# Kernel tuning notes

Measured on AMD Instinct MI355X. Metric: run time of the kernel, lower is better.

The kernel has to match this reference:

```python
import jax, jax.numpy as jnp
import numpy as np

EPS = 1e-5
NEG_INF = float('-inf')

B, L, D = 4, 1024, 1024
H = 16
HD = D // H
I = 3280  # _round_to_multiple(3.2 * 1024, 8)
WIN = 256
STD = 0.01


def rmsnorm(x, w):
    x = jnp.clip(x.astype(jnp.float32), -10000.0, 10000.0)
    rms = jnp.sqrt(jnp.maximum(jnp.mean(x * x, axis=-1, keepdims=True), EPS) + EPS)
    out = x / rms * w
    return jnp.where(jnp.isfinite(out), out, jnp.zeros_like(out))


def setup_inputs() -> dict:
    key = jax.random.key(0)
    ks = jax.random.split(key, 12)
    inp = {
        'x': jax.random.normal(ks[0], (B, L, D), dtype=jnp.float32),
        'wq_w': jax.random.normal(ks[1], (D, D), dtype=jnp.float32) * STD,
        'wq_b': jnp.zeros((D,), jnp.float32),
        'wk_w': jax.random.normal(ks[2], (D, D), dtype=jnp.float32) * STD,
        'wk_b': jnp.zeros((D,), jnp.float32),
        'wv_w': jax.random.normal(ks[3], (D, D), dtype=jnp.float32) * STD,
        'wv_b': jnp.zeros((D,), jnp.float32),
        'wo_w': jax.random.normal(ks[4], (D, D), dtype=jnp.float32) * STD,
        'wo_b': jnp.zeros((D,), jnp.float32),
        'q_norm_w': jnp.ones((HD,), jnp.float32),
        'k_norm_w': jnp.ones((HD,), jnp.float32),
        'seq_norm_w': jnp.ones((D,), jnp.float32),
        'seq_post_norm_w': jnp.ones((D,), jnp.float32),
        'ffn_norm_w': jnp.ones((D,), jnp.float32),
        'ffn_post_norm_w': jnp.ones((D,), jnp.float32),
        'w1_w': jax.random.normal(ks[5], (I, D), dtype=jnp.float32) * STD,
        'w1_b': jnp.zeros((I,), jnp.float32),
        'w2_w': jax.random.normal(ks[6], (D, I), dtype=jnp.float32) * STD,
        'w2_b': jnp.zeros((D,), jnp.float32),
        'w3_w': jax.random.normal(ks[7], (I, D), dtype=jnp.float32) * STD,
        'w3_b': jnp.zeros((I,), jnp.float32),
        'window_size': WIN,
    }
    return inp


def attention(x, wq_w, wq_b, wk_w, wk_b, wv_w, wv_b, wo_w, wo_b, q_norm_w, k_norm_w, window_size):
    b, l, d = x.shape
    x = x.astype(jnp.float32)
    q = (x @ wq_w.T + wq_b).reshape(b, l, H, HD)
    k = (x @ wk_w.T + wk_b).reshape(b, l, H, HD)
    v = (x @ wv_w.T + wv_b).reshape(b, l, H, HD)
    q = rmsnorm(q, q_norm_w)
    k = rmsnorm(k, k_norm_w)
    scale = HD ** -0.5
    scores = jnp.einsum('blhd,bmhd->bhlm', q, k) * scale
    i = jnp.arange(l)[:, None]
    j = jnp.arange(l)[None, :]
    masked = (j > i) | (i - j >= window_size)  # True => forbidden
    scores = scores + jnp.where(masked, NEG_INF, 0.0)
    p = jax.nn.softmax(scores, axis=-1)
    attn = jnp.einsum('bhlm,bmhd->blhd', p, v)
    attn = jnp.where(jnp.isfinite(attn), attn, jnp.zeros_like(attn))
    attn = attn.reshape(b, l, d)
    return attn @ wo_w.T + wo_b


def swiglu(x, w1_w, w1_b, w2_w, w2_b, w3_w, w3_b):
    x = x.astype(jnp.float32)
    z1 = x @ w1_w.T + w1_b
    z3 = x @ w3_w.T + w3_b
    return (jax.nn.silu(z1) * z3) @ w2_w.T + w2_b


def reference(x, wq_w, wq_b, wk_w, wk_b, wv_w, wv_b, wo_w, wo_b,
              q_norm_w, k_norm_w, seq_norm_w, seq_post_norm_w,
              ffn_norm_w, ffn_post_norm_w,
              w1_w, w1_b, w2_w, w2_b, w3_w, w3_b, window_size):
    # seq_norm -> attn -> seq_post_norm -> residual
    a = attention(rmsnorm(x, seq_norm_w), wq_w, wq_b, wk_w, wk_b, wv_w, wv_b,
                  wo_w, wo_b, q_norm_w, k_norm_w, window_size)
    h = x + rmsnorm(a, seq_post_norm_w)
    # ffn_norm -> ffn -> ffn_post_norm -> residual
    f = swiglu(rmsnorm(h, ffn_norm_w), w1_w, w1_b, w2_w, w2_b, w3_w, w3_b)
    return h + rmsnorm(f, ffn_post_norm_w)
```

## Files before the change

### kernel.cpp

```cpp
#include <hip/hip_runtime.h>
#include <cmath>
#include <cstdint>

typedef __bf16 bf16;
typedef bf16 bf16x4 __attribute__((ext_vector_type(4)));
typedef bf16 bf16x8 __attribute__((ext_vector_type(8)));
typedef float f32x4 __attribute__((ext_vector_type(4)));
typedef unsigned int u32;
typedef u32 u32x4 __attribute__((ext_vector_type(4)));

#define EPS 1e-5f

__device__ __forceinline__ float clipf(float v) {
    return fminf(fmaxf(v, -10000.0f), 10000.0f);
}
__device__ __forceinline__ float fin0(float v) { return isfinite(v) ? v : 0.0f; }

__device__ __forceinline__ void async_copy16(void* lds, const void* g) {
    __builtin_amdgcn_global_load_lds((__attribute__((address_space(1))) void*)(void*)g,
                                     (__attribute__((address_space(3))) void*)lds,
                                     16, 0, 0);
}

__global__ __launch_bounds__(256) void prep(const float* __restrict__ wq, const float* __restrict__ wk,
                                            const float* __restrict__ wv, const float* __restrict__ wo,
                                            bf16* __restrict__ Wq, bf16* __restrict__ Wk,
                                            bf16* __restrict__ Wv, bf16* __restrict__ Wo,
                                            const float* __restrict__ w1, const float* __restrict__ w3,
                                            bf16* __restrict__ W1p, bf16* __restrict__ W3p,
                                            const float* __restrict__ w2, bf16* __restrict__ W2p,
                                            const float* __restrict__ x, const float* __restrict__ snw,
                                            bf16* __restrict__ xn) {
    const int bid = blockIdx.x, t = threadIdx.x;
    if (bid < 4096) {
        int z = bid >> 10, r = bid & 1023;
        const float* in = (z == 0) ? wq : (z == 1) ? wk : (z == 2) ? wv : wo;
        bf16* out = (z == 0) ? Wq : (z == 1) ? Wk : (z == 2) ? Wv : Wo;
        f32x4 v = ((const f32x4*)(in + (size_t)r * 1024))[t];
        bf16x4 o = {(bf16)v[0], (bf16)v[1], (bf16)v[2], (bf16)v[3]};
        ((bf16x4*)(out + (size_t)r * 1024))[t] = o;
    } else if (bid < 10752) {
        int b2 = bid - 4096;
        int which = b2 >= 3328;
        int r = b2 - (which ? 3328 : 0);
        const float* in = which ? w3 : w1;
        bf16* out = which ? W3p : W1p;
        bf16x4 o = {(bf16)0.f, (bf16)0.f, (bf16)0.f, (bf16)0.f};
        if (r < 3280) {
            f32x4 v = ((const f32x4*)(in + (size_t)r * 1024))[t];
            o[0] = (bf16)v[0]; o[1] = (bf16)v[1]; o[2] = (bf16)v[2]; o[3] = (bf16)v[3];
        }
        ((bf16x4*)(out + (size_t)r * 1024))[t] = o;
    } else if (bid < 11776) {
        int r = bid - 10752;
        for (int c4 = t * 4; c4 < 3328; c4 += 1024) {
            bf16x4 o = {(bf16)0.f, (bf16)0.f, (bf16)0.f, (bf16)0.f};
            if (c4 + 3 < 3280) {
                f32x4 v = *(const f32x4*)(w2 + (size_t)r * 3280 + c4);
                o[0] = (bf16)v[0]; o[1] = (bf16)v[1]; o[2] = (bf16)v[2]; o[3] = (bf16)v[3];
            } else {
                #pragma unroll
                for (int j = 0; j < 4; ++j)
                    if (c4 + j < 3280) o[j] = (bf16)w2[(size_t)r * 3280 + c4 + j];
            }
            *(bf16x4*)(W2p + (size_t)r * 3328 + c4) = o;
        }
    } else {
        __shared__ float sred[4];
        int row = bid - 11776;
        f32x4 xv = ((const f32x4*)(x + (size_t)row * 1024))[t];
        f32x4 cv;
        cv[0] = clipf(xv[0]); cv[1] = clipf(xv[1]); cv[2] = clipf(xv[2]); cv[3] = clipf(xv[3]);
        float ss = cv[0]*cv[0] + cv[1]*cv[1] + cv[2]*cv[2] + cv[3]*cv[3];
        #pragma unroll
        for (int off = 32; off >= 1; off >>= 1) ss += __shfl_xor(ss, off, 64);
        if ((t & 63) == 0) sred[t >> 6] = ss;
        __syncthreads();
        float tot = sred[0] + sred[1] + sred[2] + sred[3];
        float rms = sqrtf(fmaxf(tot * (1.0f / 1024.0f), EPS) + EPS);
        f32x4 wv_ = ((const f32x4*)snw)[t];
        bf16x4 o;
        o[0] = (bf16)fin0(cv[0] / rms * wv_[0]);
        o[1] = (bf16)fin0(cv[1] / rms * wv_[1]);
        o[2] = (bf16)fin0(cv[2] / rms * wv_[2]);
        o[3] = (bf16)fin0(cv[3] / rms * wv_[3]);
        *(bf16x4*)(xn + (size_t)row * 1024 + t * 4) = o;
    }
}

__global__ __launch_bounds__(256) void gemm_qkv(const bf16* __restrict__ A,
                                                const bf16* __restrict__ B0,
                                                const bf16* __restrict__ B1,
                                                const bf16* __restrict__ B2,
                                                const float* __restrict__ g0,
                                                const float* __restrict__ g1,
                                                const float* __restrict__ g2,
                                                const float* __restrict__ qnw,
                                                const float* __restrict__ knw,
                                                bf16* __restrict__ C0,
                                                bf16* __restrict__ C1,
                                                bf16* __restrict__ VT) {
    const int z = blockIdx.z;
    const bf16* B = (z == 0) ? B0 : (z == 1) ? B1 : B2;
    const float* bias = (z == 0) ? g0 : (z == 1) ? g1 : g2;
    const float* hw = (z == 0) ? qnw : knw;

    __shared__ __align__(16) bf16 sA[2][128 * 32];
    __shared__ __align__(16) bf16 sB[2][128 * 32];
    const int tid = threadIdx.x;
    const int w = tid >> 6, lane = tid & 63;
    const int m0 = blockIdx.x * 128;
    const int n0 = blockIdx.y * 128;
    const int mwo = (w >> 1) * 64, nwo = (w & 1) * 64;
    const int r16 = lane & 15, quad = lane >> 4;
    const int kreg = quad * 8;
    const int K = 1024, N = 1024;

    f32x4 zero = {0.f, 0.f, 0.f, 0.f};
    f32x4 acc[4][4];
    #pragma unroll
    for (int i = 0; i < 4; ++i)
        #pragma unroll
        for (int j = 0; j < 4; ++j) acc[i][j] = zero;

    const int c0 = tid, c1 = tid + 256;
    const int am0 = c0 >> 2, ak0 = (c0 & 3) << 3;
    const int am1 = c1 >> 2, ak1 = (c1 & 3) << 3;

    {
        async_copy16(&sA[0][c0 * 8], &A[(size_t)(m0 + am0) * K + ak0]);
        async_copy16(&sA[0][c1 * 8], &A[(size_t)(m0 + am1) * K + ak1]);
        async_copy16(&sB[0][c0 * 8], &B[(size_t)(n0 + am0) * K + ak0]);
        async_copy16(&sB[0][c1 * 8], &B[(size_t)(n0 + am1) * K + ak1]);
    }
    for (int kt = 0; kt < 32; ++kt) {
        __syncthreads();
        const int cur = kt & 1, nxt = cur ^ 1;
        if (kt + 1 < 32) {
            const int kb = (kt + 1) << 5;
            async_copy16(&sA[nxt][c0 * 8], &A[(size_t)(m0 + am0) * K + kb + ak0]);
            async_copy16(&sA[nxt][c1 * 8], &A[(size_t)(m0 + am1) * K + kb + ak1]);
            async_copy16(&sB[nxt][c0 * 8], &B[(size_t)(n0 + am0) * K + kb + ak0]);
            async_copy16(&sB[nxt][c1 * 8], &B[(size_t)(n0 + am1) * K + kb + ak1]);
        }
        bf16x8 af[4], bfr[4];
        #pragma unroll
        for (int i = 0; i < 4; ++i) {
            af[i]  = *(const bf16x8*)&sA[cur][(mwo + i * 16 + r16) * 32 + kreg];
            bfr[i] = *(const bf16x8*)&sB[cur][(nwo + i * 16 + r16) * 32 + kreg];
        }
        #pragma unroll
        for (int mi = 0; mi < 4; ++mi)
            #pragma unroll
            for (int ni = 0; ni < 4; ++ni)
                acc[mi][ni] = __builtin_amdgcn_mfma_f32_16x16x32_bf16(af[mi], bfr[ni], acc[mi][ni], 0, 0, 0);
    }

    float bv[4];
    #pragma unroll
    for (int ni = 0; ni < 4; ++ni) bv[ni] = bias[n0 + nwo + ni * 16 + r16];

    if (z < 2) {
        bf16* C = (z == 0) ? C0 : C1;
        float nwv[4];
        #pragma unroll
        for (int ni = 0; ni < 4; ++ni) nwv[ni] = hw[ni * 16 + r16];
        #pragma unroll
        for (int mi = 0; mi < 4; ++mi) {
            #pragma unroll
            for (int r = 0; r < 4; ++r) {
                float v[4], ss = 0.0f;
                #pragma unroll
                for (int ni = 0; ni < 4; ++ni) {
                    v[ni] = clipf(acc[mi][ni][r] + bv[ni]);
                    ss += v[ni] * v[ni];
                }
                ss += __shfl_xor(ss, 1, 64);
                ss += __shfl_xor(ss, 2, 64);
                ss += __shfl_xor(ss, 4, 64);
                ss += __shfl_xor(ss, 8, 64);
                float rms = sqrtf(fmaxf(ss * (1.0f / 64.0f), EPS) + EPS);
                int row = m0 + mwo + mi * 16 + quad * 4 + r;
                #pragma unroll
                for (int ni = 0; ni < 4; ++ni) {
                    int col = n0 + nwo + ni * 16 + r16;
                    C[(size_t)row * N + col] = (bf16)fin0(v[ni] / rms * nwv[ni]);
                }
            }
        }
    } else {
        const int b_ = m0 >> 10;
        const int tokbase = (m0 & 1023) + mwo;
        #pragma unroll
        for (int ni = 0; ni < 4; ++ni) {
            int col = n0 + nwo + ni * 16 + r16;
            int h_ = col >> 6, hd = col & 63;
            bf16* dst = VT + (((size_t)b_ * 16 + h_) * 64 + hd) * 1024;
            #pragma unroll
            for (int mi = 0; mi < 4; ++mi) {
                bf16x4 pack;
                #pragma unroll
                for (int r = 0; r < 4; ++r) pack[r] = (bf16)(acc[mi][ni][r] + bv[ni]);
                *(bf16x4*)&dst[tokbase + mi * 16 + quad * 4] = pack;
            }
        }
    }
}

__global__ __launch_bounds__(256) void attn_win(const bf16* __restrict__ q,
                                                const bf16* __restrict__ k,
                                                const bf16* __restrict__ vt,
                                                const int* __restrict__ winp,
                                                bf16* __restrict__ o) {
    __shared__ __align__(16) bf16 sQ[64 * 64];
    __shared__ __align__(16) bf16 sK[64 * 64];
    __shared__ __align__(16) bf16 sVt[64 * 80];
    __shared__ __align__(16) bf16 sP[64 * 64];
    const int tid = threadIdx.x, w = tid >> 6, lane = tid & 63;
    const int qt = blockIdx.x, h = blockIdx.y, b = blockIdx.z;
    const int q0 = qt * 64;
    const int win = *winp;
    const float scale = 0.125f;
    const int r16 = lane & 15, quad = lane >> 4;

    {
        int qr0 = tid >> 3, col0 = (tid & 7) * 8;
        async_copy16(&sQ[tid * 8], &q[(((size_t)b * 1024 + q0 + qr0) * 16 + h) * 64 + col0]);
        int c1 = tid + 256;
        int qr1 = c1 >> 3, col1 = (c1 & 7) * 8;
        async_copy16(&sQ[c1 * 8], &q[(((size_t)b * 1024 + q0 + qr1) * 16 + h) * 64 + col1]);
    }
    __syncthreads();
    bf16x8 aq0 = *(const bf16x8*)&sQ[(w * 16 + r16) * 64 + quad * 8];
    bf16x8 aq1 = *(const bf16x8*)&sQ[(w * 16 + r16) * 64 + 32 + quad * 8];

    float Lr[4];
    f32x4 zero = {0.f, 0.f, 0.f, 0.f};
    f32x4 accO[4];
    #pragma unroll
    for (int r = 0; r < 4; ++r) Lr[r] = 0.0f;
    #pragma unroll
    for (int nf = 0; nf < 4; ++nf) accO[nf] = zero;

    int lo = q0 - (win - 1); if (lo < 0) lo = 0;
    const int kt0 = lo >> 6;
    const bf16* vth = vt + ((size_t)b * 16 + h) * 64 * 1024;

    for (int kt = kt0; kt <= qt; ++kt) {
        __syncthreads();
        {
            int col0 = (tid & 7) * 8;
            async_copy16(&sK[tid * 8], &k[(((size_t)b * 1024 + kt * 64 + (tid >> 3)) * 16 + h) * 64 + col0]);
            int c1 = tid + 256;
            int col1 = (c1 & 7) * 8;
            async_copy16(&sK[c1 * 8], &k[(((size_t)b * 1024 + kt * 64 + (c1 >> 3)) * 16 + h) * 64 + col1]);
        }
        #pragma unroll
        for (int c = tid; c < 512; c += 256) {
            int hd = c >> 3, koff = (c & 7) * 8;
            *(u32x4*)&sVt[hd * 80 + koff] = *(const u32x4*)&vth[(size_t)hd * 1024 + kt * 64 + koff];
        }
        __syncthreads();

        f32x4 sf[4];
        #pragma unroll
        for (int nf = 0; nf < 4; ++nf) {
            bf16x8 bk0 = *(const bf16x8*)&sK[(nf * 16 + r16) * 64 + quad * 8];
            bf16x8 bk1 = *(const bf16x8*)&sK[(nf * 16 + r16) * 64 + 32 + quad * 8];
            f32x4 accS = zero;
            accS = __builtin_amdgcn_mfma_f32_16x16x32_bf16(aq0, bk0, accS, 0, 0, 0);
            accS = __builtin_amdgcn_mfma_f32_16x16x32_bf16(aq1, bk1, accS, 0, 0, 0);
            sf[nf] = accS;
        }

        #pragma unroll
        for (int r = 0; r < 4; ++r) {
            int i = q0 + w * 16 + quad * 4 + r;
            float ps = 0.0f;
            #pragma unroll
            for (int nf = 0; nf < 4; ++nf) {
                int j = kt * 64 + nf * 16 + r16;
                bool ok = (j <= i) && (i - j < win);
                float pv = ok ? __expf(sf[nf][r] * scale - 8.0f) : 0.0f;
                ps += pv;
                sP[(w * 16 + quad * 4 + r) * 64 + nf * 16 + r16] = (bf16)pv;
            }
            Lr[r] += ps;
        }
        __syncthreads();

        bf16x8 ap0 = *(const bf16x8*)&sP[(w * 16 + r16) * 64 + quad * 8];
        bf16x8 ap1 = *(const bf16x8*)&sP[(w * 16 + r16) * 64 + 32 + quad * 8];
        #pragma unroll
        for (int nf = 0; nf < 4; ++nf) {
            bf16x8 bv0 = *(const bf16x8*)&sVt[(nf * 16 + r16) * 80 + quad * 8];
            bf16x8 bv1 = *(const bf16x8*)&sVt[(nf * 16 + r16) * 80 + 32 + quad * 8];
            accO[nf] = __builtin_amdgcn_mfma_f32_16x16x32_bf16(ap0, bv0, accO[nf], 0, 0, 0);
            accO[nf] = __builtin_amdgcn_mfma_f32_16x16x32_bf16(ap1, bv1, accO[nf], 0, 0, 0);
        }
    }

    #pragma unroll
    for (int r = 0; r < 4; ++r) {
        float l = Lr[r];
        l += __shfl_xor(l, 1, 64);
        l += __shfl_xor(l, 2, 64);
        l += __shfl_xor(l, 4, 64);
        l += __shfl_xor(l, 8, 64);
        float inv = (l > 0.0f) ? 1.0f / l : 0.0f;
        int row = q0 + w * 16 + quad * 4 + r;
        #pragma unroll
        for (int nf = 0; nf < 4; ++nf) {
            float ov = fin0(accO[nf][r] * inv);
            o[(((size_t)b * 1024 + row) * 16 + h) * 64 + nf * 16 + r16] = (bf16)ov;
        }
    }
}

__global__ __launch_bounds__(512) void gemm_sk2(const bf16* __restrict__ A,
                                                const bf16* __restrict__ B,
                                                float* __restrict__ P,
                                                int K, int Kh) {
    __shared__ __align__(16) bf16 sA[2][256 * 32];
    __shared__ __align__(16) bf16 sB[2][128 * 32];
    const int tid = threadIdx.x;
    const int w = tid >> 6, lane = tid & 63;
    const int m0 = blockIdx.x * 256, n0 = blockIdx.y * 128;
    const int mwo = (w & 3) * 64, nwo = (w >> 2) * 64;
    const int r16 = lane & 15, quad = lane >> 4, kreg = quad * 8;
    const int kbase = blockIdx.z * Kh;
    const int N = 1024;

    const int ar0 = tid >> 2,        ak0 = (tid & 3) << 3;
    const int c1 = tid + 512;
    const int ar1 = c1 >> 2,         ak1 = (c1 & 3) << 3;
    const int br = tid >> 2,         bk = (tid & 3) << 3;

    f32x4 zero = {0.f, 0.f, 0.f, 0.f};
    f32x4 acc[4][4];
    #pragma unroll
    for (int i = 0; i < 4; ++i)
        #pragma unroll
        for (int j = 0; j < 4; ++j) acc[i][j] = zero;

    {
        async_copy16(&sA[0][tid * 8], &A[(size_t)(m0 + ar0) * K + kbase + ak0]);
        async_copy16(&sA[0][c1 * 8],  &A[(size_t)(m0 + ar1) * K + kbase + ak1]);
        async_copy16(&sB[0][tid * 8], &B[(size_t)(n0 + br) * K + kbase + bk]);
    }
    const int kIters = Kh >> 5;
    for (int kt = 0; kt < kIters; ++kt) {
        __syncthreads();
        const int cur = kt & 1, nxt = cur ^ 1;
        if (kt + 1 < kIters) {
            const int kb = kbase + ((kt + 1) << 5);
            async_copy16(&sA[nxt][tid * 8], &A[(size_t)(m0 + ar0) * K + kb + ak0]);
            async_copy16(&sA[nxt][c1 * 8],  &A[(size_t)(m0 + ar1) * K + kb + ak1]);
            async_copy16(&sB[nxt][tid * 8], &B[(size_t)(n0 + br) * K + kb + bk]);
        }
        bf16x8 af[4], bfr[4];
        #pragma unroll
        for (int i = 0; i < 4; ++i) {
            af[i]  = *(const bf16x8*)&sA[cur][(mwo + i * 16 + r16) * 32 + kreg];
            bfr[i] = *(const bf16x8*)&sB[cur][(nwo + i * 16 + r16) * 32 + kreg];
        }
        #pragma unroll
        for (int mi = 0; mi < 4; ++mi)
            #pragma unroll
            for (int ni = 0; ni < 4; ++ni)
                acc[mi][ni] = __builtin_amdgcn_mfma_f32_16x16x32_bf16(af[mi], bfr[ni], acc[mi][ni], 0, 0, 0);
    }

    float* Pz = P + (size_t)blockIdx.z * 4096 * 1024;
    #pragma unroll
    for (int mi = 0; mi < 4; ++mi)
        #pragma unroll
        for (int ni = 0; ni < 4; ++ni) {
            int col = n0 + nwo + ni * 16 + r16;
            #pragma unroll
            for (int r = 0; r < 4; ++r) {
                int row = m0 + mwo + mi * 16 + quad * 4 + r;
                Pz[(size_t)row * N + col] = acc[mi][ni][r];
            }
        }
}

template <bool EMIT>
__global__ __launch_bounds__(512) void resid_norm(const float* __restrict__ xres,
                                                  const float* __restrict__ p0,
                                                  const float* __restrict__ p1,
                                                  const float* __restrict__ bias,
                                                  const float* __restrict__ wpost,
                                                  const float* __restrict__ wnext,
                                                  float* __restrict__ hout,
                                                  bf16* __restrict__ hnout) {
    __shared__ float sred[8];
    const int tid = threadIdx.x;
    const int grp = tid >> 8, t = tid & 255;
    const int w4 = (tid >> 6) & 3;
    for (int it = 0; it < 4; ++it) {
        int row = it * 1024 + blockIdx.x * 2 + grp;
        f32x4 a0 = ((const f32x4*)(p0 + (size_t)row * 1024))[t];
        f32x4 a1 = ((const f32x4*)(p1 + (size_t)row * 1024))[t];
        f32x4 bv = ((const f32x4*)bias)[t];
        f32x4 af;
        af[0] = clipf(a0[0] + a1[0] + bv[0]);
        af[1] = clipf(a0[1] + a1[1] + bv[1]);
        af[2] = clipf(a0[2] + a1[2] + bv[2]);
        af[3] = clipf(a0[3] + a1[3] + bv[3]);
        float ss = af[0]*af[0] + af[1]*af[1] + af[2]*af[2] + af[3]*af[3];
        #pragma unroll
        for (int off = 32; off >= 1; off >>= 1) ss += __shfl_xor(ss, off, 64);
        __syncthreads();
        if ((tid & 63) == 0) sred[grp * 4 + w4] = ss;
        __syncthreads();
        float tot = sred[grp*4+0] + sred[grp*4+1] + sred[grp*4+2] + sred[grp*4+3];
        float rms1 = sqrtf(fmaxf(tot * (1.0f / 1024.0f), EPS) + EPS);
        f32x4 xv = ((const f32x4*)(xres + (size_t)row * 1024))[t];
        f32x4 wp = ((const f32x4*)wpost)[t];
        f32x4 hv;
        hv[0] = xv[0] + fin0(af[0] / rms1 * wp[0]);
        hv[1] = xv[1] + fin0(af[1] / rms1 * wp[1]);
        hv[2] = xv[2] + fin0(af[2] / rms1 * wp[2]);
        hv[3] = xv[3] + fin0(af[3] / rms1 * wp[3]);
        ((f32x4*)(hout + (size_t)row * 1024))[t] = hv;
        if (EMIT) {
            f32x4 cv;
            cv[0] = clipf(hv[0]); cv[1] = clipf(hv[1]); cv[2] = clipf(hv[2]); cv[3] = clipf(hv[3]);
            float ss2 = cv[0]*cv[0] + cv[1]*cv[1] + cv[2]*cv[2] + cv[3]*cv[3];
            #pragma unroll
            for (int off = 32; off >= 1; off >>= 1) ss2 += __shfl_xor(ss2, off, 64);
            __syncthreads();
            if ((tid & 63) == 0) sred[grp * 4 + w4] = ss2;
            __syncthreads();
            float tot2 = sred[grp*4+0] + sred[grp*4+1] + sred[grp*4+2] + sred[grp*4+3];
            float rms2 = sqrtf(fmaxf(tot2 * (1.0f / 1024.0f), EPS) + EPS);
            f32x4 wn = ((const f32x4*)wnext)[t];
            bf16x4 o;
            o[0] = (bf16)fin0(cv[0] / rms2 * wn[0]);
            o[1] = (bf16)fin0(cv[1] / rms2 * wn[1]);
            o[2] = (bf16)fin0(cv[2] / rms2 * wn[2]);
            o[3] = (bf16)fin0(cv[3] / rms2 * wn[3]);
            *(bf16x4*)(hnout + (size_t)row * 1024 + t * 4) = o;
        }
    }
}

__global__ __launch_bounds__(512) void gemm_ffn1(const bf16* __restrict__ A,
                                                 const bf16* __restrict__ B1,
                                                 const bf16* __restrict__ B3,
                                                 const float* __restrict__ b1,
                                                 const float* __restrict__ b3,
                                                 bf16* __restrict__ G) {
    __shared__ __align__(16) bf16 sA[2][128 * 32];
    __shared__ __align__(16) bf16 sB1[2][128 * 32];
    __shared__ __align__(16) bf16 sB3[2][128 * 32];
    const int tid = threadIdx.x;
    const int w = tid >> 6, lane = tid & 63;
    const int m0 = blockIdx.x * 128;
    const int n0 = blockIdx.y * 128;
    const int mwo = (w >> 2) * 64, nwo = (w & 3) * 32;
    const int r16 = lane & 15, quad = lane >> 4;
    const int kreg = quad * 8;
    const int K = 1024, N = 3328;

    f32x4 zero = {0.f, 0.f, 0.f, 0.f};
    f32x4 acc1[4][2], acc3[4][2];
    #pragma unroll
    for (int i = 0; i < 4; ++i)
        #pragma unroll
        for (int j = 0; j < 2; ++j) { acc1[i][j] = zero; acc3[i][j] = zero; }

    const int arow = tid >> 2, akoff = (tid & 3) << 3;

    {
        async_copy16(&sA[0][tid * 8],  &A[(size_t)(m0 + arow) * K + akoff]);
        async_copy16(&sB1[0][tid * 8], &B1[(size_t)(n0 + arow) * K + akoff]);
        async_copy16(&sB3[0][tid * 8], &B3[(size_t)(n0 + arow) * K + akoff]);
    }
    for (int kt = 0; kt < 32; ++kt) {
        __syncthreads();
        const int cur = kt & 1, nxt = cur ^ 1;
        if (kt + 1 < 32) {
            const int kb = (kt + 1) << 5;
            async_copy16(&sA[nxt][tid * 8],  &A[(size_t)(m0 + arow) * K + kb + akoff]);
            async_copy16(&sB1[nxt][tid * 8], &B1[(size_t)(n0 + arow) * K + kb + akoff]);
            async_copy16(&sB3[nxt][tid * 8], &B3[(size_t)(n0 + arow) * K + kb + akoff]);
        }
        bf16x8 af[4], bf1[2], bf3[2];
        #pragma unroll
        for (int i = 0; i < 4; ++i)
            af[i]  = *(const bf16x8*)&sA[cur][(mwo + i * 16 + r16) * 32 + kreg];
        #pragma unroll
        for (int i = 0; i < 2; ++i) {
            bf1[i] = *(const bf16x8*)&sB1[cur][(nwo + i * 16 + r16) * 32 + kreg];
            bf3[i] = *(const bf16x8*)&sB3[cur][(nwo + i * 16 + r16) * 32 + kreg];
        }
        #pragma unroll
        for (int mi = 0; mi < 4; ++mi)
            #pragma unroll
            for (int ni = 0; ni < 2; ++ni) {
                acc1[mi][ni] = __builtin_amdgcn_mfma_f32_16x16x32_bf16(af[mi], bf1[ni], acc1[mi][ni], 0, 0, 0);
                acc3[mi][ni] = __builtin_amdgcn_mfma_f32_16x16x32_bf16(af[mi], bf3[ni], acc3[mi][ni], 0, 0, 0);
            }
    }

    #pragma unroll
    for (int ni = 0; ni < 2; ++ni) {
        int col = n0 + nwo + ni * 16 + r16;
        float bv1 = (col < 3280) ? b1[col] : 0.0f;
        float bv3 = (col < 3280) ? b3[col] : 0.0f;
        #pragma unroll
        for (int mi = 0; mi < 4; ++mi) {
            #pragma unroll
            for (int r = 0; r < 4; ++r) {
                int row = m0 + mwo + mi * 16 + quad * 4 + r;
                float z1 = acc1[mi][ni][r] + bv1;
                float z3 = acc3[mi][ni][r] + bv3;
                float s = z1 / (1.0f + __expf(-z1));
                G[(size_t)row * N + col] = (bf16)(s * z3);
            }
        }
    }
}

extern "C" void kernel_launch(void* const* d_in, const int* in_sizes, int n_in,
                              void* d_out, int out_size, void* d_ws, size_t ws_size,
                              hipStream_t stream) {
    const float* x       = (const float*)d_in[0];
    const float* wq_w    = (const float*)d_in[1];
    const float* wq_b    = (const float*)d_in[2];
    const float* wk_w    = (const float*)d_in[3];
    const float* wk_b    = (const float*)d_in[4];
    const float* wv_w    = (const float*)d_in[5];
    const float* wv_b    = (const float*)d_in[6];
    const float* wo_w    = (const float*)d_in[7];
    const float* wo_b    = (const float*)d_in[8];
    const float* q_norm_w= (const float*)d_in[9];
    const float* k_norm_w= (const float*)d_in[10];
    const float* seq_norm_w      = (const float*)d_in[11];
    const float* seq_post_norm_w = (const float*)d_in[12];
    const float* ffn_norm_w      = (const float*)d_in[13];
    const float* ffn_post_norm_w = (const float*)d_in[14];
    const float* w1_w    = (const float*)d_in[15];
    const float* w1_b    = (const float*)d_in[16];
    const float* w2_w    = (const float*)d_in[17];
    const float* w2_b    = (const float*)d_in[18];
    const float* w3_w    = (const float*)d_in[19];
    const float* w3_b    = (const float*)d_in[20];
    const int*   winp    = (const int*)d_in[21];
    float* out = (float*)d_out;

    const size_t SZ_W   = 2097152;
    const size_t SZ_WP  = 6815744;
    const size_t SZ_ACT = 8388608;
    const size_t SZ_H   = 16777216;
    const size_t SZ_P   = 33554432;

    char* p = (char*)d_ws;
    bf16* Wq  = (bf16*)p; p += SZ_W;
    bf16* Wk  = (bf16*)p; p += SZ_W;
    bf16* Wv  = (bf16*)p; p += SZ_W;
    bf16* Wo  = (bf16*)p; p += SZ_W;
    bf16* W1p = (bf16*)p; p += SZ_WP;
    bf16* W3p = (bf16*)p; p += SZ_WP;
    bf16* W2p = (bf16*)p; p += SZ_WP;
    float* h  = (float*)p; p += SZ_H;
    bf16* hn  = (bf16*)p; p += SZ_ACT;
    float* part = (float*)p; p += SZ_P;
    float* part1 = part + (size_t)4096 * 1024;
    char* regionA = p;
    bf16* xn    = (bf16*)(regionA);
    bf16* qb    = (bf16*)(regionA + 1 * SZ_ACT);
    bf16* kb    = (bf16*)(regionA + 2 * SZ_ACT);
    bf16* vtb   = (bf16*)(regionA + 3 * SZ_ACT);
    bf16* attnb = (bf16*)(regionA + 4 * SZ_ACT);
    bf16* g     = (bf16*)(regionA);

    prep<<<dim3(15872), dim3(256), 0, stream>>>(wq_w, wk_w, wv_w, wo_w, Wq, Wk, Wv, Wo,
                                                w1_w, w3_w, W1p, W3p, w2_w, W2p,
                                                x, seq_norm_w, xn);

    gemm_qkv<<<dim3(32, 8, 3), dim3(256), 0, stream>>>(xn, Wq, Wk, Wv, wq_b, wk_b, wv_b,
                                                       q_norm_w, k_norm_w, qb, kb, vtb);

    attn_win<<<dim3(16, 16, 4), dim3(256), 0, stream>>>(qb, kb, vtb, winp, attnb);

    gemm_sk2<<<dim3(16, 8, 2), dim3(512), 0, stream>>>(attnb, Wo, part, 1024, 512);

    resid_norm<true><<<dim3(512), dim3(512), 0, stream>>>(x, part, part1, wo_b,
                                                          seq_post_norm_w, ffn_norm_w, h, hn);

    gemm_ffn1<<<dim3(32, 26), dim3(512), 0, stream>>>(hn, W1p, W3p, w1_b, w3_b, g);

    gemm_sk2<<<dim3(16, 8, 2), dim3(512), 0, stream>>>(g, W2p, part, 3328, 1664);

    resid_norm<false><<<dim3(512), dim3(512), 0, stream>>>(h, part, part1, w2_b,
                                                           ffn_post_norm_w, nullptr, out, nullptr);
}
```

Baseline: 371.0 us.

## Interleave W1/W3 weights and rewrite FFN1 GEMM with 256x256 tiles and phased pipeline

The prep kernel now interleaves W1 and W3 rows in blocks of 16 into one combined weight matrix, so FFN1 runs as a single GEMM with N=6656. The new FFN1 kernel uses 256x256 block tiles with K-tiles of 64, XOR-swizzled LDS layout, staggered async loads for A and B halves interleaved with MFMA phases, s_setprio around MFMA bursts, and a grouped block-index swizzle for L2 locality. It is meant to raise data reuse per LDS load and overlap global loads with compute, in exchange for more registers and LDS per block and hand-tuned waitcnt ordering that could be fragile.

```diff
diff --git a/kernel.cpp b/kernel.cpp
--- a/kernel.cpp
+++ b/kernel.cpp
@@ -27,7 +27,7 @@
                                             bf16* __restrict__ Wq, bf16* __restrict__ Wk,
                                             bf16* __restrict__ Wv, bf16* __restrict__ Wo,
                                             const float* __restrict__ w1, const float* __restrict__ w3,
-                                            bf16* __restrict__ W1p, bf16* __restrict__ W3p,
+                                            bf16* __restrict__ Wf,
                                             const float* __restrict__ w2, bf16* __restrict__ W2p,
                                             const float* __restrict__ x, const float* __restrict__ snw,
                                             bf16* __restrict__ xn) {
@@ -40,17 +40,15 @@
         bf16x4 o = {(bf16)v[0], (bf16)v[1], (bf16)v[2], (bf16)v[3]};
         ((bf16x4*)(out + (size_t)r * 1024))[t] = o;
     } else if (bid < 10752) {
-        int b2 = bid - 4096;
-        int which = b2 >= 3328;
-        int r = b2 - (which ? 3328 : 0);
-        const float* in = which ? w3 : w1;
-        bf16* out = which ? W3p : W1p;
+        int ri = bid - 4096;
+        int lc = ((ri >> 5) << 4) + (ri & 15);
+        const float* in = ((ri >> 4) & 1) ? w3 : w1;
         bf16x4 o = {(bf16)0.f, (bf16)0.f, (bf16)0.f, (bf16)0.f};
-        if (r < 3280) {
-            f32x4 v = ((const f32x4*)(in + (size_t)r * 1024))[t];
+        if (lc < 3280) {
+            f32x4 v = ((const f32x4*)(in + (size_t)lc * 1024))[t];
             o[0] = (bf16)v[0]; o[1] = (bf16)v[1]; o[2] = (bf16)v[2]; o[3] = (bf16)v[3];
         }
-        ((bf16x4*)(out + (size_t)r * 1024))[t] = o;
+        ((bf16x4*)(Wf + (size_t)ri * 1024))[t] = o;
     } else if (bid < 11776) {
         int r = bid - 10752;
         for (int c4 = t * 4; c4 < 3328; c4 += 1024) {
@@ -446,79 +444,119 @@
     }
 }
 
-__global__ __launch_bounds__(512) void gemm_ffn1(const bf16* __restrict__ A,
-                                                 const bf16* __restrict__ B1,
-                                                 const bf16* __restrict__ B3,
-                                                 const float* __restrict__ b1,
-                                                 const float* __restrict__ b3,
-                                                 bf16* __restrict__ G) {
-    __shared__ __align__(16) bf16 sA[2][128 * 32];
-    __shared__ __align__(16) bf16 sB1[2][128 * 32];
-    __shared__ __align__(16) bf16 sB3[2][128 * 32];
+template <int MB>
+__device__ __forceinline__ void mphase(const bf16* Ah, const bf16x8 (&breg)[4][2],
+                                       f32x4 (&acc)[8][4], int r16, int koff0, int koff1) {
+    const bf16* pa0 = &Ah[(MB * 16 + r16) * 64];
+    const bf16* pa1 = &Ah[((MB + 1) * 16 + r16) * 64];
+    bf16x8 a00 = *(const bf16x8*)&pa0[koff0];
+    bf16x8 a01 = *(const bf16x8*)&pa0[koff1];
+    bf16x8 a10 = *(const bf16x8*)&pa1[koff0];
+    bf16x8 a11 = *(const bf16x8*)&pa1[koff1];
+    __builtin_amdgcn_s_setprio(1);
+    #pragma unroll
+    for (int n = 0; n < 4; ++n) {
+        acc[MB][n]     = __builtin_amdgcn_mfma_f32_16x16x32_bf16(a00, breg[n][0], acc[MB][n], 0, 0, 0);
+        acc[MB][n]     = __builtin_amdgcn_mfma_f32_16x16x32_bf16(a01, breg[n][1], acc[MB][n], 0, 0, 0);
+        acc[MB + 1][n] = __builtin_amdgcn_mfma_f32_16x16x32_bf16(a10, breg[n][0], acc[MB + 1][n], 0, 0, 0);
+        acc[MB + 1][n] = __builtin_amdgcn_mfma_f32_16x16x32_bf16(a11, breg[n][1], acc[MB + 1][n], 0, 0, 0);
+    }
+    __builtin_amdgcn_s_setprio(0);
+}
+
+__global__ __launch_bounds__(512, 2) void gemm_ffn1_8ph(const bf16* __restrict__ A,
+                                                        const bf16* __restrict__ Wf,
+                                                        const float* __restrict__ b1,
+                                                        const float* __restrict__ b3,
+                                                        bf16* __restrict__ G) {
+    __shared__ __align__(16) bf16 sA[2][2][128 * 64];
+    __shared__ __align__(16) bf16 sB[2][2][128 * 64];
     const int tid = threadIdx.x;
     const int w = tid >> 6, lane = tid & 63;
-    const int m0 = blockIdx.x * 128;
-    const int n0 = blockIdx.y * 128;
-    const int mwo = (w >> 2) * 64, nwo = (w & 3) * 32;
+    const int wr = w >> 2, wc = w & 3;
     const int r16 = lane & 15, quad = lane >> 4;
-    const int kreg = quad * 8;
-    const int K = 1024, N = 3328;
-
-    f32x4 zero = {0.f, 0.f, 0.f, 0.f};
-    f32x4 acc1[4][2], acc3[4][2];
-    #pragma unroll
-    for (int i = 0; i < 4; ++i)
-        #pragma unroll
-        for (int j = 0; j < 2; ++j) { acc1[i][j] = zero; acc3[i][j] = zero; }
-
-    const int arow = tid >> 2, akoff = (tid & 3) << 3;
-
-    {
-        async_copy16(&sA[0][tid * 8],  &A[(size_t)(m0 + arow) * K + akoff]);
-        async_copy16(&sB1[0][tid * 8], &B1[(size_t)(n0 + arow) * K + akoff]);
-        async_copy16(&sB3[0][tid * 8], &B3[(size_t)(n0 + arow) * K + akoff]);
-    }
-    for (int kt = 0; kt < 32; ++kt) {
-        __syncthreads();
-        const int cur = kt & 1, nxt = cur ^ 1;
-        if (kt + 1 < 32) {
-            const int kb = (kt + 1) << 5;
-            async_copy16(&sA[nxt][tid * 8],  &A[(size_t)(m0 + arow) * K + kb + akoff]);
-            async_copy16(&sB1[nxt][tid * 8], &B1[(size_t)(n0 + arow) * K + kb + akoff]);
-            async_copy16(&sB3[nxt][tid * 8], &B3[(size_t)(n0 + arow) * K + kb + akoff]);
-        }
-        bf16x8 af[4], bf1[2], bf3[2];
-        #pragma unroll
-        for (int i = 0; i < 4; ++i)
-            af[i]  = *(const bf16x8*)&sA[cur][(mwo + i * 16 + r16) * 32 + kreg];
-        #pragma unroll
-        for (int i = 0; i < 2; ++i) {
-            bf1[i] = *(const bf16x8*)&sB1[cur][(nwo + i * 16 + r16) * 32 + kreg];
-            bf3[i] = *(const bf16x8*)&sB3[cur][(nwo + i * 16 + r16) * 32 + kreg];
-        }
-        #pragma unroll
-        for (int mi = 0; mi < 4; ++mi)
-            #pragma unroll
-            for (int ni = 0; ni < 2; ++ni) {
-                acc1[mi][ni] = __builtin_amdgcn_mfma_f32_16x16x32_bf16(af[mi], bf1[ni], acc1[mi][ni], 0, 0, 0);
-                acc3[mi][ni] = __builtin_amdgcn_mfma_f32_16x16x32_bf16(af[mi], bf3[ni], acc3[mi][ni], 0, 0, 0);
-            }
-    }
-
-    #pragma unroll
-    for (int ni = 0; ni < 2; ++ni) {
-        int col = n0 + nwo + ni * 16 + r16;
-        float bv1 = (col < 3280) ? b1[col] : 0.0f;
-        float bv3 = (col < 3280) ? b3[col] : 0.0f;
-        #pragma unroll
-        for (int mi = 0; mi < 4; ++mi) {
-            #pragma unroll
-            for (int r = 0; r < 4; ++r) {
-                int row = m0 + mwo + mi * 16 + quad * 4 + r;
-                float z1 = acc1[mi][ni][r] + bv1;
-                float z3 = acc3[mi][ni][r] + bv3;
+
+    const int flat = blockIdx.x;
+    const int swb = (flat & 7) * 52 + (flat >> 3);
+    const int bm = swb & 15, bn = swb >> 4;
+    const int m0 = bm * 256;
+    const int n0i = bn * 256;
+
+    const int swz = r16 & 7;
+    const int koff0 = ((quad ^ swz) << 3);
+    const int koff1 = (((quad + 4) ^ swz) << 3);
+
+    const int sr0 = tid >> 3, sr1 = sr0 + 64;
+    const int sk0 = (((tid & 7) ^ (sr0 & 7)) << 3);
+
+    const bf16* aSrc0 = A + (size_t)m0 * 1024;
+    const bf16* aSrc1 = A + (size_t)(m0 + 128) * 1024;
+    const bf16* bSrc0 = Wf + (size_t)n0i * 1024;
+    const bf16* bSrc1 = Wf + (size_t)(n0i + 128) * 1024;
+
+#define STAGE(dst, src, ktile) do {                                                        \
+        async_copy16(&(dst)[tid * 8],         (src) + (size_t)sr0 * 1024 + (ktile) * 64 + sk0); \
+        async_copy16(&(dst)[(tid + 512) * 8], (src) + (size_t)sr1 * 1024 + (ktile) * 64 + sk0); \
+    } while (0)
+
+    f32x4 acc[8][4];
+    #pragma unroll
+    for (int i = 0; i < 8; ++i)
+        #pragma unroll
+        for (int j = 0; j < 4; ++j) acc[i][j] = (f32x4){0.f, 0.f, 0.f, 0.f};
+
+    STAGE(sB[0][0], bSrc0, 0); STAGE(sB[0][1], bSrc1, 0);
+    STAGE(sA[0][0], aSrc0, 0); STAGE(sA[0][1], aSrc1, 0);
+    STAGE(sB[1][0], bSrc0, 1); STAGE(sB[1][1], bSrc1, 1);
+
+    for (int t = 0; t < 16; ++t) {
+        const int cur = t & 1, nxt = cur ^ 1;
+        const bf16* Ah = &sA[cur][wr][0];
+        const bf16* Bh = &sB[cur][wc >> 1][0];
+        const int rbB = (wc & 1) << 6;
+        bf16x8 breg[4][2];
+
+        __builtin_amdgcn_s_barrier();
+        if (t + 1 < 16) {
+            STAGE(sA[nxt][0], aSrc0, t + 1);
+            STAGE(sA[nxt][1], aSrc1, t + 1);
+        }
+        if (t == 15) { asm volatile("s_waitcnt vmcnt(0)" ::: "memory"); }
+        else         { asm volatile("s_waitcnt vmcnt(8)" ::: "memory"); }
+        #pragma unroll
+        for (int n = 0; n < 4; ++n) {
+            const bf16* p = &Bh[(rbB + n * 16 + r16) * 64];
+            breg[n][0] = *(const bf16x8*)&p[koff0];
+            breg[n][1] = *(const bf16x8*)&p[koff1];
+        }
+        mphase<0>(Ah, breg, acc, r16, koff0, koff1);
+
+        __builtin_amdgcn_s_barrier();
+        if (t + 2 < 16) STAGE(sB[cur][0], bSrc0, t + 2);
+        mphase<2>(Ah, breg, acc, r16, koff0, koff1);
+
+        __builtin_amdgcn_s_barrier();
+        if (t + 2 < 16) STAGE(sB[cur][1], bSrc1, t + 2);
+        mphase<4>(Ah, breg, acc, r16, koff0, koff1);
+
+        mphase<6>(Ah, breg, acc, r16, koff0, koff1);
+    }
+#undef STAGE
+
+    #pragma unroll
+    for (int m = 0; m < 8; ++m) {
+        #pragma unroll
+        for (int p = 0; p < 2; ++p) {
+            int col = (bn * 8 + wc * 2 + p) * 16 + r16;
+            float bb1 = (col < 3280) ? b1[col] : 0.0f;
+            float bb3 = (col < 3280) ? b3[col] : 0.0f;
+            #pragma unroll
+            for (int rr = 0; rr < 4; ++rr) {
+                int row = m0 + wr * 128 + m * 16 + quad * 4 + rr;
+                float z1 = acc[m][2 * p][rr] + bb1;
+                float z3 = acc[m][2 * p + 1][rr] + bb3;
                 float s = z1 / (1.0f + __expf(-z1));
-                G[(size_t)row * N + col] = (bf16)(s * z3);
+                G[(size_t)row * 3328 + col] = (bf16)(s * z3);
             }
         }
     }
@@ -562,8 +600,7 @@
     bf16* Wk  = (bf16*)p; p += SZ_W;
     bf16* Wv  = (bf16*)p; p += SZ_W;
     bf16* Wo  = (bf16*)p; p += SZ_W;
-    bf16* W1p = (bf16*)p; p += SZ_WP;
-    bf16* W3p = (bf16*)p; p += SZ_WP;
+    bf16* Wfp = (bf16*)p; p += 2 * SZ_WP;
     bf16* W2p = (bf16*)p; p += SZ_WP;
     float* h  = (float*)p; p += SZ_H;
     bf16* hn  = (bf16*)p; p += SZ_ACT;
@@ -578,7 +615,7 @@
     bf16* g     = (bf16*)(regionA);
 
     prep<<<dim3(15872), dim3(256), 0, stream>>>(wq_w, wk_w, wv_w, wo_w, Wq, Wk, Wv, Wo,
-                                                w1_w, w3_w, W1p, W3p, w2_w, W2p,
+                                                w1_w, w3_w, Wfp, w2_w, W2p,
                                                 x, seq_norm_w, xn);
 
     gemm_qkv<<<dim3(32, 8, 3), dim3(256), 0, stream>>>(xn, Wq, Wk, Wv, wq_b, wk_b, wv_b,
@@ -591,7 +628,7 @@
     resid_norm<true><<<dim3(512), dim3(512), 0, stream>>>(x, part, part1, wo_b,
                                                           seq_post_norm_w, ffn_norm_w, h, hn);
 
-    gemm_ffn1<<<dim3(32, 26), dim3(512), 0, stream>>>(hn, W1p, W3p, w1_b, w3_b, g);
+    gemm_ffn1_8ph<<<dim3(416), dim3(512), 0, stream>>>(hn, Wfp, w1_b, w3_b, g);
 
     gemm_sk2<<<dim3(16, 8, 2), dim3(512), 0, stream>>>(g, W2p, part, 3328, 1664);
 
```

Result: slower. 391.6 us (+5.5%).

## Overlap Wo/FFN weight conversion with QKV GEMM via extra grid slice

Applied to the files above, without the earlier changes.

Moves the fp32-to-bf16 conversion of Wo, W1, W3 and W2 out of the prep kernel into a new z=0 slice of the QKV GEMM grid. 256 blocks stride over the 8704 weight rows while the other slices run the QKV GEMM. This shrinks the prep kernel and lets the bandwidth-bound conversion run alongside compute-bound GEMM work. The risk is that the conversion blocks hold CUs and compete for memory bandwidth with the GEMM, and that the z indexing has to be remapped correctly for Q, K and V.

```diff
diff --git a/kernel.cpp b/kernel.cpp
--- a/kernel.cpp
+++ b/kernel.cpp
@@ -23,51 +23,22 @@
 }
 
 __global__ __launch_bounds__(256) void prep(const float* __restrict__ wq, const float* __restrict__ wk,
-                                            const float* __restrict__ wv, const float* __restrict__ wo,
+                                            const float* __restrict__ wv,
                                             bf16* __restrict__ Wq, bf16* __restrict__ Wk,
-                                            bf16* __restrict__ Wv, bf16* __restrict__ Wo,
-                                            const float* __restrict__ w1, const float* __restrict__ w3,
-                                            bf16* __restrict__ W1p, bf16* __restrict__ W3p,
-                                            const float* __restrict__ w2, bf16* __restrict__ W2p,
+                                            bf16* __restrict__ Wv,
                                             const float* __restrict__ x, const float* __restrict__ snw,
                                             bf16* __restrict__ xn) {
     const int bid = blockIdx.x, t = threadIdx.x;
-    if (bid < 4096) {
+    if (bid < 3072) {
         int z = bid >> 10, r = bid & 1023;
-        const float* in = (z == 0) ? wq : (z == 1) ? wk : (z == 2) ? wv : wo;
-        bf16* out = (z == 0) ? Wq : (z == 1) ? Wk : (z == 2) ? Wv : Wo;
+        const float* in = (z == 0) ? wq : (z == 1) ? wk : wv;
+        bf16* out = (z == 0) ? Wq : (z == 1) ? Wk : Wv;
         f32x4 v = ((const f32x4*)(in + (size_t)r * 1024))[t];
         bf16x4 o = {(bf16)v[0], (bf16)v[1], (bf16)v[2], (bf16)v[3]};
         ((bf16x4*)(out + (size_t)r * 1024))[t] = o;
-    } else if (bid < 10752) {
-        int b2 = bid - 4096;
-        int which = b2 >= 3328;
-        int r = b2 - (which ? 3328 : 0);
-        const float* in = which ? w3 : w1;
-        bf16* out = which ? W3p : W1p;
-        bf16x4 o = {(bf16)0.f, (bf16)0.f, (bf16)0.f, (bf16)0.f};
-        if (r < 3280) {
-            f32x4 v = ((const f32x4*)(in + (size_t)r * 1024))[t];
-            o[0] = (bf16)v[0]; o[1] = (bf16)v[1]; o[2] = (bf16)v[2]; o[3] = (bf16)v[3];
-        }
-        ((bf16x4*)(out + (size_t)r * 1024))[t] = o;
-    } else if (bid < 11776) {
-        int r = bid - 10752;
-        for (int c4 = t * 4; c4 < 3328; c4 += 1024) {
-            bf16x4 o = {(bf16)0.f, (bf16)0.f, (bf16)0.f, (bf16)0.f};
-            if (c4 + 3 < 3280) {
-                f32x4 v = *(const f32x4*)(w2 + (size_t)r * 3280 + c4);
-                o[0] = (bf16)v[0]; o[1] = (bf16)v[1]; o[2] = (bf16)v[2]; o[3] = (bf16)v[3];
-            } else {
-                #pragma unroll
-                for (int j = 0; j < 4; ++j)
-                    if (c4 + j < 3280) o[j] = (bf16)w2[(size_t)r * 3280 + c4 + j];
-            }
-            *(bf16x4*)(W2p + (size_t)r * 3328 + c4) = o;
-        }
     } else {
         __shared__ float sred[4];
-        int row = bid - 11776;
+        int row = bid - 3072;
         f32x4 xv = ((const f32x4*)(x + (size_t)row * 1024))[t];
         f32x4 cv;
         cv[0] = clipf(xv[0]); cv[1] = clipf(xv[1]); cv[2] = clipf(xv[2]); cv[3] = clipf(xv[3]);
@@ -99,15 +70,61 @@
                                                 const float* __restrict__ knw,
                                                 bf16* __restrict__ C0,
                                                 bf16* __restrict__ C1,
-                                                bf16* __restrict__ VT) {
+                                                bf16* __restrict__ VT,
+                                                const float* __restrict__ wo,
+                                                const float* __restrict__ w1,
+                                                const float* __restrict__ w3,
+                                                const float* __restrict__ w2,
+                                                bf16* __restrict__ Wo,
+                                                bf16* __restrict__ W1p,
+                                                bf16* __restrict__ W3p,
+                                                bf16* __restrict__ W2p) {
     const int z = blockIdx.z;
-    const bf16* B = (z == 0) ? B0 : (z == 1) ? B1 : B2;
-    const float* bias = (z == 0) ? g0 : (z == 1) ? g1 : g2;
-    const float* hw = (z == 0) ? qnw : knw;
+    const int tid = threadIdx.x;
+
+    if (z == 0) {
+        const int cid = blockIdx.y * 32 + blockIdx.x;
+        for (int u = cid; u < 8704; u += 256) {
+            if (u < 1024) {
+                f32x4 v = ((const f32x4*)(wo + (size_t)u * 1024))[tid];
+                bf16x4 o = {(bf16)v[0], (bf16)v[1], (bf16)v[2], (bf16)v[3]};
+                ((bf16x4*)(Wo + (size_t)u * 1024))[tid] = o;
+            } else if (u < 7680) {
+                int which = u >= 4352;
+                int r = u - (which ? 4352 : 1024);
+                const float* in = which ? w3 : w1;
+                bf16* out = which ? W3p : W1p;
+                bf16x4 o = {(bf16)0.f, (bf16)0.f, (bf16)0.f, (bf16)0.f};
+                if (r < 3280) {
+                    f32x4 v = ((const f32x4*)(in + (size_t)r * 1024))[tid];
+                    o[0] = (bf16)v[0]; o[1] = (bf16)v[1]; o[2] = (bf16)v[2]; o[3] = (bf16)v[3];
+                }
+                ((bf16x4*)(out + (size_t)r * 1024))[tid] = o;
+            } else {
+                int r = u - 7680;
+                for (int c4 = tid * 4; c4 < 3328; c4 += 1024) {
+                    bf16x4 o = {(bf16)0.f, (bf16)0.f, (bf16)0.f, (bf16)0.f};
+                    if (c4 + 3 < 3280) {
+                        f32x4 v = *(const f32x4*)(w2 + (size_t)r * 3280 + c4);
+                        o[0] = (bf16)v[0]; o[1] = (bf16)v[1]; o[2] = (bf16)v[2]; o[3] = (bf16)v[3];
+                    } else {
+                        #pragma unroll
+                        for (int j = 0; j < 4; ++j)
+                            if (c4 + j < 3280) o[j] = (bf16)w2[(size_t)r * 3280 + c4 + j];
+                    }
+                    *(bf16x4*)(W2p + (size_t)r * 3328 + c4) = o;
+                }
+            }
+        }
+        return;
+    }
+
+    const bf16* B = (z == 1) ? B0 : (z == 2) ? B1 : B2;
+    const float* bias = (z == 1) ? g0 : (z == 2) ? g1 : g2;
+    const float* hw = (z == 1) ? qnw : knw;
 
     __shared__ __align__(16) bf16 sA[2][128 * 32];
     __shared__ __align__(16) bf16 sB[2][128 * 32];
-    const int tid = threadIdx.x;
     const int w = tid >> 6, lane = tid & 63;
     const int m0 = blockIdx.x * 128;
     const int n0 = blockIdx.y * 128;
@@ -160,8 +177,8 @@
     #pragma unroll
     for (int ni = 0; ni < 4; ++ni) bv[ni] = bias[n0 + nwo + ni * 16 + r16];
 
-    if (z < 2) {
-        bf16* C = (z == 0) ? C0 : C1;
+    if (z < 3) {
+        bf16* C = (z == 1) ? C0 : C1;
         float nwv[4];
         #pragma unroll
         for (int ni = 0; ni < 4; ++ni) nwv[ni] = hw[ni * 16 + r16];
@@ -577,12 +594,13 @@
     bf16* attnb = (bf16*)(regionA + 4 * SZ_ACT);
     bf16* g     = (bf16*)(regionA);
 
-    prep<<<dim3(15872), dim3(256), 0, stream>>>(wq_w, wk_w, wv_w, wo_w, Wq, Wk, Wv, Wo,
-                                                w1_w, w3_w, W1p, W3p, w2_w, W2p,
-                                                x, seq_norm_w, xn);
-
-    gemm_qkv<<<dim3(32, 8, 3), dim3(256), 0, stream>>>(xn, Wq, Wk, Wv, wq_b, wk_b, wv_b,
-                                                       q_norm_w, k_norm_w, qb, kb, vtb);
+    prep<<<dim3(7168), dim3(256), 0, stream>>>(wq_w, wk_w, wv_w, Wq, Wk, Wv,
+                                               x, seq_norm_w, xn);
+
+    gemm_qkv<<<dim3(32, 8, 4), dim3(256), 0, stream>>>(xn, Wq, Wk, Wv, wq_b, wk_b, wv_b,
+                                                       q_norm_w, k_norm_w, qb, kb, vtb,
+                                                       wo_w, w1_w, w3_w, w2_w,
+                                                       Wo, W1p, W3p, W2p);
 
     attn_win<<<dim3(16, 16, 4), dim3(256), 0, stream>>>(qb, kb, vtb, winp, attnb);
 
```

Measured after the change: 393.6 us. 1.06x slower.

## Fuse Q/K/V projections into one GEMM kernel sharing the A tile

Applied to the files above, without the earlier changes.

Replaces the three-way z-split QKV GEMM with a single 512-thread kernel that loads each A tile once and multiplies it against the Q, K and V weight tiles together. Each of the 8 warps covers a 32x64 sub-tile with three accumulator sets. The goal is to cut redundant activation loads and the number of launched blocks. The cost is more LDS per block (four double-buffered tiles), more accumulator registers per thread, and only 256 blocks instead of 768, which may reduce occupancy and parallelism.

```diff
diff --git a/kernel.cpp b/kernel.cpp
--- a/kernel.cpp
+++ b/kernel.cpp
@@ -88,91 +88,96 @@
     }
 }
 
-__global__ __launch_bounds__(256) void gemm_qkv(const bf16* __restrict__ A,
-                                                const bf16* __restrict__ B0,
-                                                const bf16* __restrict__ B1,
-                                                const bf16* __restrict__ B2,
-                                                const float* __restrict__ g0,
-                                                const float* __restrict__ g1,
-                                                const float* __restrict__ g2,
-                                                const float* __restrict__ qnw,
-                                                const float* __restrict__ knw,
-                                                bf16* __restrict__ C0,
-                                                bf16* __restrict__ C1,
-                                                bf16* __restrict__ VT) {
-    const int z = blockIdx.z;
-    const bf16* B = (z == 0) ? B0 : (z == 1) ? B1 : B2;
-    const float* bias = (z == 0) ? g0 : (z == 1) ? g1 : g2;
-    const float* hw = (z == 0) ? qnw : knw;
-
+__global__ __launch_bounds__(512) void gemm_qkv3(const bf16* __restrict__ A,
+                                                 const bf16* __restrict__ Bq,
+                                                 const bf16* __restrict__ Bk,
+                                                 const bf16* __restrict__ Bv,
+                                                 const float* __restrict__ biq,
+                                                 const float* __restrict__ bik,
+                                                 const float* __restrict__ biv,
+                                                 const float* __restrict__ qnw,
+                                                 const float* __restrict__ knw,
+                                                 bf16* __restrict__ Cq,
+                                                 bf16* __restrict__ Ck,
+                                                 bf16* __restrict__ VT) {
     __shared__ __align__(16) bf16 sA[2][128 * 32];
-    __shared__ __align__(16) bf16 sB[2][128 * 32];
+    __shared__ __align__(16) bf16 sBq[2][128 * 32];
+    __shared__ __align__(16) bf16 sBk[2][128 * 32];
+    __shared__ __align__(16) bf16 sBv[2][128 * 32];
     const int tid = threadIdx.x;
     const int w = tid >> 6, lane = tid & 63;
     const int m0 = blockIdx.x * 128;
     const int n0 = blockIdx.y * 128;
-    const int mwo = (w >> 1) * 64, nwo = (w & 1) * 64;
+    const int mwo = (w >> 1) * 32;
+    const int nwo = (w & 1) * 64;
     const int r16 = lane & 15, quad = lane >> 4;
     const int kreg = quad * 8;
     const int K = 1024, N = 1024;
 
     f32x4 zero = {0.f, 0.f, 0.f, 0.f};
-    f32x4 acc[4][4];
-    #pragma unroll
-    for (int i = 0; i < 4; ++i)
-        #pragma unroll
-        for (int j = 0; j < 4; ++j) acc[i][j] = zero;
-
-    const int c0 = tid, c1 = tid + 256;
-    const int am0 = c0 >> 2, ak0 = (c0 & 3) << 3;
-    const int am1 = c1 >> 2, ak1 = (c1 & 3) << 3;
+    f32x4 aq[2][4], ak[2][4], av[2][4];
+    #pragma unroll
+    for (int i = 0; i < 2; ++i)
+        #pragma unroll
+        for (int j = 0; j < 4; ++j) { aq[i][j] = zero; ak[i][j] = zero; av[i][j] = zero; }
+
+    const int arow = tid >> 2, akoff = (tid & 3) << 3;
 
     {
-        async_copy16(&sA[0][c0 * 8], &A[(size_t)(m0 + am0) * K + ak0]);
-        async_copy16(&sA[0][c1 * 8], &A[(size_t)(m0 + am1) * K + ak1]);
-        async_copy16(&sB[0][c0 * 8], &B[(size_t)(n0 + am0) * K + ak0]);
-        async_copy16(&sB[0][c1 * 8], &B[(size_t)(n0 + am1) * K + ak1]);
+        async_copy16(&sA[0][tid * 8],  &A[(size_t)(m0 + arow) * K + akoff]);
+        async_copy16(&sBq[0][tid * 8], &Bq[(size_t)(n0 + arow) * K + akoff]);
+        async_copy16(&sBk[0][tid * 8], &Bk[(size_t)(n0 + arow) * K + akoff]);
+        async_copy16(&sBv[0][tid * 8], &Bv[(size_t)(n0 + arow) * K + akoff]);
     }
     for (int kt = 0; kt < 32; ++kt) {
         __syncthreads();
         const int cur = kt & 1, nxt = cur ^ 1;
         if (kt + 1 < 32) {
             const int kb = (kt + 1) << 5;
-            async_copy16(&sA[nxt][c0 * 8], &A[(size_t)(m0 + am0) * K + kb + ak0]);
-            async_copy16(&sA[nxt][c1 * 8], &A[(size_t)(m0 + am1) * K + kb + ak1]);
-            async_copy16(&sB[nxt][c0 * 8], &B[(size_t)(n0 + am0) * K + kb + ak0]);
-            async_copy16(&sB[nxt][c1 * 8], &B[(size_t)(n0 + am1) * K + kb + ak1]);
-        }
-        bf16x8 af[4], bfr[4];
+            async_copy16(&sA[nxt][tid * 8],  &A[(size_t)(m0 + arow) * K + kb + akoff]);
+            async_copy16(&sBq[nxt][tid * 8], &Bq[(size_t)(n0 + arow) * K + kb + akoff]);
+            async_copy16(&sBk[nxt][tid * 8], &Bk[(size_t)(n0 + arow) * K + kb + akoff]);
+            async_copy16(&sBv[nxt][tid * 8], &Bv[(size_t)(n0 + arow) * K + kb + akoff]);
+        }
+        bf16x8 af[2], bq_[4], bk_[4], bv_[4];
+        #pragma unroll
+        for (int i = 0; i < 2; ++i)
+            af[i] = *(const bf16x8*)&sA[cur][(mwo + i * 16 + r16) * 32 + kreg];
         #pragma unroll
         for (int i = 0; i < 4; ++i) {
-            af[i]  = *(const bf16x8*)&sA[cur][(mwo + i * 16 + r16) * 32 + kreg];
-            bfr[i] = *(const bf16x8*)&sB[cur][(nwo + i * 16 + r16) * 32 + kreg];
-        }
-        #pragma unroll
-        for (int mi = 0; mi < 4; ++mi)
-            #pragma unroll
-            for (int ni = 0; ni < 4; ++ni)
-                acc[mi][ni] = __builtin_amdgcn_mfma_f32_16x16x32_bf16(af[mi], bfr[ni], acc[mi][ni], 0, 0, 0);
-    }
-
-    float bv[4];
-    #pragma unroll
-    for (int ni = 0; ni < 4; ++ni) bv[ni] = bias[n0 + nwo + ni * 16 + r16];
-
-    if (z < 2) {
-        bf16* C = (z == 0) ? C0 : C1;
-        float nwv[4];
-        #pragma unroll
-        for (int ni = 0; ni < 4; ++ni) nwv[ni] = hw[ni * 16 + r16];
-        #pragma unroll
-        for (int mi = 0; mi < 4; ++mi) {
+            bq_[i] = *(const bf16x8*)&sBq[cur][(nwo + i * 16 + r16) * 32 + kreg];
+            bk_[i] = *(const bf16x8*)&sBk[cur][(nwo + i * 16 + r16) * 32 + kreg];
+            bv_[i] = *(const bf16x8*)&sBv[cur][(nwo + i * 16 + r16) * 32 + kreg];
+        }
+        #pragma unroll
+        for (int mi = 0; mi < 2; ++mi)
+            #pragma unroll
+            for (int ni = 0; ni < 4; ++ni) {
+                aq[mi][ni] = __builtin_amdgcn_mfma_f32_16x16x32_bf16(af[mi], bq_[ni], aq[mi][ni], 0, 0, 0);
+                ak[mi][ni] = __builtin_amdgcn_mfma_f32_16x16x32_bf16(af[mi], bk_[ni], ak[mi][ni], 0, 0, 0);
+                av[mi][ni] = __builtin_amdgcn_mfma_f32_16x16x32_bf16(af[mi], bv_[ni], av[mi][ni], 0, 0, 0);
+            }
+    }
+
+    float nwq[4], nwk[4], bvq[4], bvk[4], bvv[4];
+    #pragma unroll
+    for (int ni = 0; ni < 4; ++ni) {
+        int col = n0 + nwo + ni * 16 + r16;
+        bvq[ni] = biq[col]; bvk[ni] = bik[col]; bvv[ni] = biv[col];
+        nwq[ni] = qnw[ni * 16 + r16]; nwk[ni] = knw[ni * 16 + r16];
+    }
+    #pragma unroll
+    for (int s = 0; s < 2; ++s) {
+        bf16* C = s ? Ck : Cq;
+        #pragma unroll
+        for (int mi = 0; mi < 2; ++mi) {
             #pragma unroll
             for (int r = 0; r < 4; ++r) {
                 float v[4], ss = 0.0f;
                 #pragma unroll
                 for (int ni = 0; ni < 4; ++ni) {
-                    v[ni] = clipf(acc[mi][ni][r] + bv[ni]);
+                    float a = s ? ak[mi][ni][r] : aq[mi][ni][r];
+                    v[ni] = clipf(a + (s ? bvk[ni] : bvq[ni]));
                     ss += v[ni] * v[ni];
                 }
                 ss += __shfl_xor(ss, 1, 64);
@@ -184,11 +189,13 @@
                 #pragma unroll
                 for (int ni = 0; ni < 4; ++ni) {
                     int col = n0 + nwo + ni * 16 + r16;
-                    C[(size_t)row * N + col] = (bf16)fin0(v[ni] / rms * nwv[ni]);
+                    float nw = s ? nwk[ni] : nwq[ni];
+                    C[(size_t)row * N + col] = (bf16)fin0(v[ni] / rms * nw);
                 }
             }
         }
-    } else {
+    }
+    {
         const int b_ = m0 >> 10;
         const int tokbase = (m0 & 1023) + mwo;
         #pragma unroll
@@ -197,10 +204,10 @@
             int h_ = col >> 6, hd = col & 63;
             bf16* dst = VT + (((size_t)b_ * 16 + h_) * 64 + hd) * 1024;
             #pragma unroll
-            for (int mi = 0; mi < 4; ++mi) {
+            for (int mi = 0; mi < 2; ++mi) {
                 bf16x4 pack;
                 #pragma unroll
-                for (int r = 0; r < 4; ++r) pack[r] = (bf16)(acc[mi][ni][r] + bv[ni]);
+                for (int r = 0; r < 4; ++r) pack[r] = (bf16)(av[mi][ni][r] + bvv[ni]);
                 *(bf16x4*)&dst[tokbase + mi * 16 + quad * 4] = pack;
             }
         }
@@ -581,8 +588,8 @@
                                                 w1_w, w3_w, W1p, W3p, w2_w, W2p,
                                                 x, seq_norm_w, xn);
 
-    gemm_qkv<<<dim3(32, 8, 3), dim3(256), 0, stream>>>(xn, Wq, Wk, Wv, wq_b, wk_b, wv_b,
-                                                       q_norm_w, k_norm_w, qb, kb, vtb);
+    gemm_qkv3<<<dim3(32, 8), dim3(512), 0, stream>>>(xn, Wq, Wk, Wv, wq_b, wk_b, wv_b,
+                                                     q_norm_w, k_norm_w, qb, kb, vtb);
 
     attn_win<<<dim3(16, 16, 4), dim3(256), 0, stream>>>(qb, kb, vtb, winp, attnb);
 
```

After: 380.3 us. +2.5%, slower.
